# Kernel tuning notes

Hardware: AMD Instinct MI355X
Metric: run time of the kernel (lower is better)

Reference implementation:

```python
import jax, jax.numpy as jnp
import numpy as np

D = 768
H = 12
DH = D // H  # 64


def setup_inputs() -> dict:
    key = jax.random.key(0)
    ks = jax.random.split(key, 7)
    B, N = 16, 1024
    sequences = jax.random.normal(ks[0], (B, N, D), dtype=jnp.float32)
    s = 1.0 / np.sqrt(DH)
    # per-head torch Linear params: weight [out, in] = [DH, DH], bias [DH]
    Wq = jax.random.uniform(ks[1], (H, DH, DH), jnp.float32, -s, s)
    Wk = jax.random.uniform(ks[2], (H, DH, DH), jnp.float32, -s, s)
    Wv = jax.random.uniform(ks[3], (H, DH, DH), jnp.float32, -s, s)
    bq = jax.random.uniform(ks[4], (H, DH), jnp.float32, -s, s)
    bk = jax.random.uniform(ks[5], (H, DH), jnp.float32, -s, s)
    bv = jax.random.uniform(ks[6], (H, DH), jnp.float32, -s, s)
    return {"sequences": sequences, "Wq": Wq, "Wk": Wk, "Wv": Wv,
            "bq": bq, "bk": bk, "bv": bv}


def reference(sequences, Wq, Wk, Wv, bq, bk, bv):
    B, N, _ = sequences.shape
    x = sequences.reshape(B, N, H, DH)  # head slices of the feature dim
    # torch Linear: y = x @ W.T + b  -> einsum over the 'in' axis of W
    q = jnp.einsum('bnhd,hed->bnhe', x, Wq) + bq
    k = jnp.einsum('bnhd,hed->bnhe', x, Wk) + bk
    v = jnp.einsum('bnhd,hed->bnhe', x, Wv) + bv
    scores = jnp.einsum('bnhe,bmhe->bhnm', q, k) / jnp.sqrt(jnp.float32(DH))
    attn = jax.nn.softmax(scores, axis=-1)  # [B,H,N,N]
    out = jnp.einsum('bhnm,bmhe->bnhe', attn, v)
    return out.reshape(B, N, H * DH)  # hstack of per-head outputs
```

## Files before the change

### kernel.cpp

```cpp
#include <hip/hip_runtime.h>


#define NH 12
#define DHEAD 64
#define BB 16
#define NSEQ 1024
#define DMODEL 768
#define LSTR 72
#define QSCALE 0.18033688f

typedef unsigned short u16;
typedef unsigned int u32;
typedef u16 u16x8 __attribute__((ext_vector_type(8)));
typedef u16 u16x4 __attribute__((ext_vector_type(4)));
typedef __bf16 bf16x8 __attribute__((ext_vector_type(8)));
typedef float f32x4 __attribute__((ext_vector_type(4)));

union Frag { u16x8 u; bf16x8 b; };

__device__ __forceinline__ float fast_exp2(float x) {
#if __has_builtin(__builtin_amdgcn_exp2f)
    return __builtin_amdgcn_exp2f(x);
#else
    return exp2f(x);
#endif
}

__device__ __forceinline__ u16 f2bf(float f) {
    union { __bf16 h; u16 u; } c; c.h = (__bf16)f; return c.u;
}

__device__ __forceinline__ u16x8 cvt8(const float* __restrict__ p) {
    f32x4 a = *(const f32x4*)p;
    f32x4 b = *(const f32x4*)(p + 4);
    Frag r;
    r.b[0] = (__bf16)a[0]; r.b[1] = (__bf16)a[1]; r.b[2] = (__bf16)a[2]; r.b[3] = (__bf16)a[3];
    r.b[4] = (__bf16)b[0]; r.b[5] = (__bf16)b[1]; r.b[6] = (__bf16)b[2]; r.b[7] = (__bf16)b[3];
    return r.u;
}

__global__ __launch_bounds__(256) void wcvt_kernel(
    const float* __restrict__ Wq, const float* __restrict__ Wk,
    const float* __restrict__ Wv, u16* __restrict__ Wb)
{
    const int bx = blockIdx.x;
    const int m = bx / 24;
    const int off = (bx % 24) * 2048 + threadIdx.x * 8;
    const float* srcs[3] = { Wq, Wk, Wv };
    *(u16x8*)(Wb + m * 49152 + off) = cvt8(srcs[m] + off);
}

__global__ __launch_bounds__(256) void kv_kernel(
    const float* __restrict__ x,
    const u16*  __restrict__ Wb,
    const float* __restrict__ bk, const float* __restrict__ bv,
    u16* __restrict__ Ko,
    u16* __restrict__ Vt)
{
    __shared__ __align__(16) u16 w_lds[2][64 * LSTR];
    __shared__ __align__(16) u16 x_lds[128 * LSTR];

    const int bid = blockIdx.x;
    const int h     = bid % NH;
    const int chunk = (bid / NH) & 7;
    const int b     = bid / (NH * 8);

    const int t = threadIdx.x, lane = t & 63, wave = t >> 6;
    const int qd = lane >> 4, lm = lane & 15;

    {
        const int row = t >> 2, d0 = (t & 3) * 16;
#pragma unroll
        for (int m = 0; m < 2; m++) {
            const u16* s = Wb + (1 + m) * 49152 + h * 4096 + row * 64 + d0;
            *(u16x8*)&w_lds[m][row * LSTR + d0]     = *(const u16x8*)s;
            *(u16x8*)&w_lds[m][row * LSTR + d0 + 8] = *(const u16x8*)(s + 8);
        }
        const int xr = t >> 1, xd = (t & 1) * 32;
        const float* s = x + ((size_t)(b * NSEQ + chunk * 128 + xr)) * DMODEL + h * DHEAD + xd;
#pragma unroll
        for (int i = 0; i < 4; i++)
            *(u16x8*)&x_lds[xr * LSTR + xd + i * 8] = cvt8(s + i * 8);
    }
    __syncthreads();

    Frag xfrag[2][2];
#pragma unroll
    for (int mt = 0; mt < 2; mt++)
#pragma unroll
        for (int kk = 0; kk < 2; kk++)
            xfrag[mt][kk].u = *(const u16x8*)&x_lds[(wave * 32 + mt * 16 + lm) * LSTR + kk * 32 + qd * 8];

    u16* tx = &x_lds[wave * 32 * LSTR];
    const int key_base = chunk * 128 + wave * 32;

#pragma unroll
    for (int et = 0; et < 4; et++) {
        Frag wfrag[2];
#pragma unroll
        for (int kk = 0; kk < 2; kk++)
            wfrag[kk].u = *(const u16x8*)&w_lds[0][(et * 16 + lm) * LSTR + kk * 32 + qd * 8];
        f32x4 acc0 = {0.f,0.f,0.f,0.f}, acc1 = {0.f,0.f,0.f,0.f};
#pragma unroll
        for (int kk = 0; kk < 2; kk++) {
            acc0 = __builtin_amdgcn_mfma_f32_16x16x32_bf16(wfrag[kk].b, xfrag[0][kk].b, acc0, 0, 0, 0);
            acc1 = __builtin_amdgcn_mfma_f32_16x16x32_bf16(wfrag[kk].b, xfrag[1][kk].b, acc1, 0, 0, 0);
        }
        f32x4 b4 = *(const f32x4*)&bk[h * DHEAD + et * 16 + qd * 4];
        u16x4 o0, o1;
#pragma unroll
        for (int r = 0; r < 4; r++) {
            o0[r] = f2bf(acc0[r] + b4[r]);
            o1[r] = f2bf(acc1[r] + b4[r]);
        }
        *(u16x4*)&tx[lm * LSTR + et * 16 + qd * 4]        = o0;
        *(u16x4*)&tx[(16 + lm) * LSTR + et * 16 + qd * 4] = o1;
    }
    {
        const size_t base_out = ((size_t)(b * NH + h) * NSEQ + key_base) * DHEAD;
#pragma unroll
        for (int j = 0; j < 4; j++) {
            const int row = j * 8 + (lane >> 3), col = (lane & 7) * 8;
            u16x8 v = *(const u16x8*)&tx[row * LSTR + col];
            *(u16x8*)(Ko + base_out + (size_t)row * DHEAD + col) = v;
        }
    }

    const size_t vt_base = ((size_t)(b * NH + h)) * DHEAD * NSEQ;
#pragma unroll
    for (int et = 0; et < 4; et++) {
        Frag wvfrag[2];
#pragma unroll
        for (int kk = 0; kk < 2; kk++)
            wvfrag[kk].u = *(const u16x8*)&w_lds[1][(et * 16 + lm) * LSTR + kk * 32 + qd * 8];
        const float bvv = bv[h * DHEAD + et * 16 + lm];
#pragma unroll
        for (int mt = 0; mt < 2; mt++) {
            f32x4 acc = {0.f,0.f,0.f,0.f};
#pragma unroll
            for (int kk = 0; kk < 2; kk++)
                acc = __builtin_amdgcn_mfma_f32_16x16x32_bf16(xfrag[mt][kk].b, wvfrag[kk].b, acc, 0, 0, 0);
            u16x4 o;
#pragma unroll
            for (int r = 0; r < 4; r++) o[r] = f2bf(acc[r] + bvv);
            *(u16x4*)(Vt + vt_base + (size_t)(et * 16 + lm) * NSEQ + key_base + mt * 16 + qd * 4) = o;
        }
    }
}

__global__ __launch_bounds__(256, 2) void attn_kernel(
    const float* __restrict__ x, const u16* __restrict__ Wb,
    const float* __restrict__ bq,
    const u16* __restrict__ K, const u16* __restrict__ Vt,
    float* __restrict__ out)
{
    __shared__ __align__(16) u16 k_lds[64 * LSTR];
    __shared__ __align__(16) u16 vt_lds[64 * LSTR];
    __shared__ __align__(16) u16 p_lds[4][16 * LSTR];

    const int bid = blockIdx.x;
    const int bh = bid % 192;
    const int qt = bid / 192;
    const int h = bh % NH, b = bh / NH;

    const int t = threadIdx.x, lane = t & 63, wave = t >> 6;
    const int qd = lane >> 4, lm = lane & 15;
    const size_t bh_off = (size_t)bh * NSEQ * DHEAD;
    const int tb = qt * 256;

    {
        const int row = t >> 2, d0 = (t & 3) * 16;
        const u16* wq = Wb + h * 4096 + row * 64 + d0;
        *(u16x8*)&k_lds[row * LSTR + d0]     = *(const u16x8*)wq;
        *(u16x8*)&k_lds[row * LSTR + d0 + 8] = *(const u16x8*)(wq + 8);
    }
    __syncthreads();

    Frag qfrag[4][2];
    {
        const int xrow = lane >> 2, xd0 = (lane & 3) * 16;
#pragma unroll
        for (int mtl = 0; mtl < 4; mtl++) {
            const float* xs = x + ((size_t)(b * NSEQ + tb + wave * 64 + mtl * 16 + xrow)) * DMODEL
                              + h * DHEAD + xd0;
            *(u16x8*)&p_lds[wave][xrow * LSTR + xd0]     = cvt8(xs);
            *(u16x8*)&p_lds[wave][xrow * LSTR + xd0 + 8] = cvt8(xs + 8);
            Frag xB[2];
#pragma unroll
            for (int kk = 0; kk < 2; kk++)
                xB[kk].u = *(const u16x8*)&p_lds[wave][lm * LSTR + kk * 32 + qd * 8];
#pragma unroll
            for (int et = 0; et < 4; et++) {
                Frag wqA[2];
#pragma unroll
                for (int kk = 0; kk < 2; kk++)
                    wqA[kk].u = *(const u16x8*)&k_lds[(et * 16 + lm) * LSTR + kk * 32 + qd * 8];
                f32x4 acc = {0.f,0.f,0.f,0.f};
#pragma unroll
                for (int kk = 0; kk < 2; kk++)
                    acc = __builtin_amdgcn_mfma_f32_16x16x32_bf16(wqA[kk].b, xB[kk].b, acc, 0, 0, 0);
                f32x4 b4 = *(const f32x4*)&bq[h * DHEAD + et * 16 + qd * 4];
                u16x4 o;
#pragma unroll
                for (int r = 0; r < 4; r++) o[r] = f2bf((acc[r] + b4[r]) * QSCALE);
                *(u16x4*)&p_lds[wave][lm * LSTR + et * 16 + qd * 4] = o;
            }
#pragma unroll
            for (int kk = 0; kk < 2; kk++)
                qfrag[mtl][kk].u = *(const u16x8*)&p_lds[wave][lm * LSTR + kk * 32 + qd * 8];
        }
    }

    f32x4 o_acc[4][4] = {};
    f32x4 rsum = {0.f, 0.f, 0.f, 0.f};

    const u16* kb = K  + bh_off;
    const u16* vb = Vt + bh_off;

    const int srow = t >> 2, sd0 = (t & 3) * 16;

    u16x8 kreg0, kreg1, vreg0, vreg1;
    {
        const u16* sk = kb + (size_t)srow * DHEAD + sd0;
        kreg0 = *(const u16x8*)sk; kreg1 = *(const u16x8*)(sk + 8);
        const u16* sv = vb + (size_t)srow * NSEQ + sd0;
        vreg0 = *(const u16x8*)sv; vreg1 = *(const u16x8*)(sv + 8);
    }

#pragma unroll 1
    for (int it = 0; it < NSEQ / 64; it++) {
        __syncthreads();
        *(u16x8*)&k_lds[srow * LSTR + sd0]      = kreg0;
        *(u16x8*)&k_lds[srow * LSTR + sd0 + 8]  = kreg1;
        *(u16x8*)&vt_lds[srow * LSTR + sd0]     = vreg0;
        *(u16x8*)&vt_lds[srow * LSTR + sd0 + 8] = vreg1;
        __syncthreads();

        if (it + 1 < NSEQ / 64) {
            const u16* sk = kb + (size_t)((it + 1) * 64 + srow) * DHEAD + sd0;
            kreg0 = *(const u16x8*)sk; kreg1 = *(const u16x8*)(sk + 8);
            const u16* sv = vb + (size_t)srow * NSEQ + (it + 1) * 64 + sd0;
            vreg0 = *(const u16x8*)sv; vreg1 = *(const u16x8*)(sv + 8);
        }

        Frag kfrag[4][2];
#pragma unroll
        for (int kt = 0; kt < 4; kt++)
#pragma unroll
            for (int kk = 0; kk < 2; kk++)
                kfrag[kt][kk].u = *(const u16x8*)&k_lds[(kt * 16 + lm) * LSTR + kk * 32 + qd * 8];

        Frag pfrag[4][2];
#pragma unroll
        for (int mt = 0; mt < 4; mt++) {
            f32x4 st[4];
#pragma unroll
            for (int kt = 0; kt < 4; kt++) {
                f32x4 a = {0.f,0.f,0.f,0.f};
#pragma unroll
                for (int kk = 0; kk < 2; kk++)
                    a = __builtin_amdgcn_mfma_f32_16x16x32_bf16(kfrag[kt][kk].b, qfrag[mt][kk].b, a, 0, 0, 0);
                st[kt] = a;
            }
            float rs = 0.f;
#pragma unroll
            for (int kt = 0; kt < 4; kt++) {
                u16x4 pk;
#pragma unroll
                for (int r = 0; r < 4; r++) {
                    float p = fast_exp2(st[kt][r]);
                    rs += p;
                    pk[r] = f2bf(p);
                }
                *(u16x4*)&p_lds[wave][lm * LSTR + kt * 16 + qd * 4] = pk;
            }
            rsum[mt] += rs;
#pragma unroll
            for (int kk = 0; kk < 2; kk++)
                pfrag[mt][kk].u = *(const u16x8*)&p_lds[wave][lm * LSTR + kk * 32 + qd * 8];
        }

#pragma unroll
        for (int dt = 0; dt < 4; dt++) {
            Frag vfrag[2];
#pragma unroll
            for (int kk = 0; kk < 2; kk++)
                vfrag[kk].u = *(const u16x8*)&vt_lds[(dt * 16 + lm) * LSTR + kk * 32 + qd * 8];
#pragma unroll
            for (int kk = 0; kk < 2; kk++)
#pragma unroll
                for (int mt = 0; mt < 4; mt++)
                    o_acc[mt][dt] = __builtin_amdgcn_mfma_f32_16x16x32_bf16(pfrag[mt][kk].b, vfrag[kk].b, o_acc[mt][dt], 0, 0, 0);
        }
    }

#pragma unroll
    for (int mt = 0; mt < 4; mt++) {
        float s = rsum[mt];
        s += __shfl_xor(s, 16);
        s += __shfl_xor(s, 32);
        float inv = 1.f / s;
        float inv4[4];
#pragma unroll
        for (int r = 0; r < 4; r++) inv4[r] = __shfl(inv, qd * 4 + r);
#pragma unroll
        for (int dt = 0; dt < 4; dt++) {
            const int e = dt * 16 + lm;
#pragma unroll
            for (int r = 0; r < 4; r++) {
                const int n_tok = tb + wave * 64 + mt * 16 + qd * 4 + r;
                out[((size_t)(b * NSEQ + n_tok)) * DMODEL + h * DHEAD + e] =
                    o_acc[mt][dt][r] * inv4[r];
            }
        }
    }
}

extern "C" void kernel_launch(void* const* d_in, const int* in_sizes, int n_in,
                              void* d_out, int out_size, void* d_ws, size_t ws_size,
                              hipStream_t stream) {
    const float* x  = (const float*)d_in[0];
    const float* Wq = (const float*)d_in[1];
    const float* Wk = (const float*)d_in[2];
    const float* Wv = (const float*)d_in[3];
    const float* bq = (const float*)d_in[4];
    const float* bk = (const float*)d_in[5];
    const float* bv = (const float*)d_in[6];
    float* out = (float*)d_out;

    const size_t KV_ELEMS = (size_t)BB * NH * NSEQ * DHEAD;
    u16* Kw  = (u16*)d_ws;
    u16* Vtw = Kw + KV_ELEMS;
    u16* Wb  = Vtw + KV_ELEMS;

    wcvt_kernel<<<72, 256, 0, stream>>>(Wq, Wk, Wv, Wb);
    kv_kernel<<<BB * 8 * NH, 256, 0, stream>>>(x, Wb, bk, bv, Kw, Vtw);
    attn_kernel<<<(NSEQ / 256) * BB * NH, 256, 0, stream>>>(x, Wb, bq, Kw, Vtw, out);
}
```

Baseline: 96.83 us.

## Double-buffer K/V LDS, swizzle layout, and use permlane swaps instead of P round-trip

Replaces the padded single-buffer K/V shared-memory tiles with XOR-style swizzled, double-buffered tiles. This cuts the two barriers per iteration to one and lets loads for tile it+2 overlap compute on tile it. The P (softmax probabilities) and Q fragments are no longer written to and re-read from LDS. They are rearranged in registers with permlane32/permlane16 swap intrinsics, which removes the per-wave LDS scratch and its traffic. The cost is more LDS for double buffering, a dependency on the gfx950 permlane builtins, and a risk of getting the fragment lane mapping wrong.

After: 99.13 us. +2.4%, slower.

```diff
diff --git a/kernel.cpp b/kernel.cpp
--- a/kernel.cpp
+++ b/kernel.cpp
@@ -15,8 +15,9 @@
 typedef u16 u16x4 __attribute__((ext_vector_type(4)));
 typedef __bf16 bf16x8 __attribute__((ext_vector_type(8)));
 typedef float f32x4 __attribute__((ext_vector_type(4)));
-
-union Frag { u16x8 u; bf16x8 b; };
+typedef int i32x2 __attribute__((ext_vector_type(2)));
+
+union Frag { u16x8 u; bf16x8 b; u32 w[4]; };
 
 __device__ __forceinline__ float fast_exp2(float x) {
 #if __has_builtin(__builtin_amdgcn_exp2f)
@@ -28,6 +29,10 @@
 
 __device__ __forceinline__ u16 f2bf(float f) {
     union { __bf16 h; u16 u; } c; c.h = (__bf16)f; return c.u;
+}
+
+__device__ __forceinline__ u32 pk2(float lo, float hi) {
+    return (u32)f2bf(lo) | ((u32)f2bf(hi) << 16);
 }
 
 __device__ __forceinline__ u16x8 cvt8(const float* __restrict__ p) {
@@ -37,6 +42,16 @@
     r.b[0] = (__bf16)a[0]; r.b[1] = (__bf16)a[1]; r.b[2] = (__bf16)a[2]; r.b[3] = (__bf16)a[3];
     r.b[4] = (__bf16)b[0]; r.b[5] = (__bf16)b[1]; r.b[6] = (__bf16)b[2]; r.b[7] = (__bf16)b[3];
     return r.u;
+}
+
+__device__ __forceinline__ int sw(int row, int slot) {
+    return (row << 6) + (((slot + row) & 7) << 3);
+}
+
+__device__ __forceinline__ void lane4_shuffle(u32 a0, u32 a1, u32& wlo, u32& whi) {
+    i32x2 t = __builtin_amdgcn_permlane32_swap((int)a0, (int)a1, false, false);
+    i32x2 r = __builtin_amdgcn_permlane16_swap(t[0], t[1], false, false);
+    wlo = (u32)r[0]; whi = (u32)r[1];
 }
 
 __global__ __launch_bounds__(256) void wcvt_kernel(
@@ -154,9 +169,8 @@
     const u16* __restrict__ K, const u16* __restrict__ Vt,
     float* __restrict__ out)
 {
-    __shared__ __align__(16) u16 k_lds[64 * LSTR];
-    __shared__ __align__(16) u16 vt_lds[64 * LSTR];
-    __shared__ __align__(16) u16 p_lds[4][16 * LSTR];
+    __shared__ __align__(16) u16 k_lds[2][64 * 64];
+    __shared__ __align__(16) u16 v_lds[2][64 * 64];
 
     const int bid = blockIdx.x;
     const int bh = bid % 192;
@@ -168,87 +182,81 @@
     const size_t bh_off = (size_t)bh * NSEQ * DHEAD;
     const int tb = qt * 256;
 
-    {
-        const int row = t >> 2, d0 = (t & 3) * 16;
-        const u16* wq = Wb + h * 4096 + row * 64 + d0;
-        *(u16x8*)&k_lds[row * LSTR + d0]     = *(const u16x8*)wq;
-        *(u16x8*)&k_lds[row * LSTR + d0 + 8] = *(const u16x8*)(wq + 8);
+    const u16* kb = K  + bh_off;
+    const u16* vb = Vt + bh_off;
+
+    const int srow = t >> 2, sc = t & 3;
+
+    {
+        const u16* wq = Wb + h * 4096 + srow * 64 + sc * 16;
+        *(u16x8*)&k_lds[0][sw(srow, sc * 2)]     = *(const u16x8*)wq;
+        *(u16x8*)&k_lds[0][sw(srow, sc * 2 + 1)] = *(const u16x8*)(wq + 8);
+    }
+
+    u16x8 kreg0, kreg1, vreg0, vreg1;
+    {
+        const u16* sk = kb + (size_t)srow * DHEAD + sc * 16;
+        kreg0 = *(const u16x8*)sk; kreg1 = *(const u16x8*)(sk + 8);
+        const u16* sv = vb + (size_t)srow * NSEQ + sc * 16;
+        vreg0 = *(const u16x8*)sv; vreg1 = *(const u16x8*)(sv + 8);
     }
     __syncthreads();
 
     Frag qfrag[4][2];
-    {
-        const int xrow = lane >> 2, xd0 = (lane & 3) * 16;
-#pragma unroll
-        for (int mtl = 0; mtl < 4; mtl++) {
-            const float* xs = x + ((size_t)(b * NSEQ + tb + wave * 64 + mtl * 16 + xrow)) * DMODEL
-                              + h * DHEAD + xd0;
-            *(u16x8*)&p_lds[wave][xrow * LSTR + xd0]     = cvt8(xs);
-            *(u16x8*)&p_lds[wave][xrow * LSTR + xd0 + 8] = cvt8(xs + 8);
-            Frag xB[2];
-#pragma unroll
-            for (int kk = 0; kk < 2; kk++)
-                xB[kk].u = *(const u16x8*)&p_lds[wave][lm * LSTR + kk * 32 + qd * 8];
-#pragma unroll
-            for (int et = 0; et < 4; et++) {
-                Frag wqA[2];
-#pragma unroll
-                for (int kk = 0; kk < 2; kk++)
-                    wqA[kk].u = *(const u16x8*)&k_lds[(et * 16 + lm) * LSTR + kk * 32 + qd * 8];
-                f32x4 acc = {0.f,0.f,0.f,0.f};
-#pragma unroll
-                for (int kk = 0; kk < 2; kk++)
-                    acc = __builtin_amdgcn_mfma_f32_16x16x32_bf16(wqA[kk].b, xB[kk].b, acc, 0, 0, 0);
-                f32x4 b4 = *(const f32x4*)&bq[h * DHEAD + et * 16 + qd * 4];
-                u16x4 o;
-#pragma unroll
-                for (int r = 0; r < 4; r++) o[r] = f2bf((acc[r] + b4[r]) * QSCALE);
-                *(u16x4*)&p_lds[wave][lm * LSTR + et * 16 + qd * 4] = o;
-            }
-#pragma unroll
-            for (int kk = 0; kk < 2; kk++)
-                qfrag[mtl][kk].u = *(const u16x8*)&p_lds[wave][lm * LSTR + kk * 32 + qd * 8];
-        }
-    }
+#pragma unroll
+    for (int mtl = 0; mtl < 4; mtl++) {
+        const float* xs = x + ((size_t)(b * NSEQ + tb + wave * 64 + mtl * 16 + lm)) * DMODEL
+                          + h * DHEAD + qd * 8;
+        Frag xB[2];
+        xB[0].u = cvt8(xs);
+        xB[1].u = cvt8(xs + 32);
+        u32 Ap[4], Bp[4];
+#pragma unroll
+        for (int et = 0; et < 4; et++) {
+            Frag wqA[2];
+#pragma unroll
+            for (int kk = 0; kk < 2; kk++)
+                wqA[kk].u = *(const u16x8*)&k_lds[0][sw(et * 16 + lm, kk * 4 + qd)];
+            f32x4 acc = {0.f,0.f,0.f,0.f};
+#pragma unroll
+            for (int kk = 0; kk < 2; kk++)
+                acc = __builtin_amdgcn_mfma_f32_16x16x32_bf16(wqA[kk].b, xB[kk].b, acc, 0, 0, 0);
+            f32x4 b4 = *(const f32x4*)&bq[h * DHEAD + et * 16 + qd * 4];
+            Ap[et] = pk2((acc[0] + b4[0]) * QSCALE, (acc[1] + b4[1]) * QSCALE);
+            Bp[et] = pk2((acc[2] + b4[2]) * QSCALE, (acc[3] + b4[3]) * QSCALE);
+        }
+#pragma unroll
+        for (int kk = 0; kk < 2; kk++) {
+            lane4_shuffle(Ap[2 * kk], Ap[2 * kk + 1], qfrag[mtl][kk].w[0], qfrag[mtl][kk].w[2]);
+            lane4_shuffle(Bp[2 * kk], Bp[2 * kk + 1], qfrag[mtl][kk].w[1], qfrag[mtl][kk].w[3]);
+        }
+    }
+
+    *(u16x8*)&k_lds[1][sw(srow, sc * 2)]     = kreg0;
+    *(u16x8*)&k_lds[1][sw(srow, sc * 2 + 1)] = kreg1;
+    *(u16x8*)&v_lds[1][sw(srow, sc * 2)]     = vreg0;
+    *(u16x8*)&v_lds[1][sw(srow, sc * 2 + 1)] = vreg1;
+    {
+        const u16* sk = kb + (size_t)(64 + srow) * DHEAD + sc * 16;
+        kreg0 = *(const u16x8*)sk; kreg1 = *(const u16x8*)(sk + 8);
+        const u16* sv = vb + (size_t)srow * NSEQ + 64 + sc * 16;
+        vreg0 = *(const u16x8*)sv; vreg1 = *(const u16x8*)(sv + 8);
+    }
+    __syncthreads();
 
     f32x4 o_acc[4][4] = {};
     f32x4 rsum = {0.f, 0.f, 0.f, 0.f};
 
-    const u16* kb = K  + bh_off;
-    const u16* vb = Vt + bh_off;
-
-    const int srow = t >> 2, sd0 = (t & 3) * 16;
-
-    u16x8 kreg0, kreg1, vreg0, vreg1;
-    {
-        const u16* sk = kb + (size_t)srow * DHEAD + sd0;
-        kreg0 = *(const u16x8*)sk; kreg1 = *(const u16x8*)(sk + 8);
-        const u16* sv = vb + (size_t)srow * NSEQ + sd0;
-        vreg0 = *(const u16x8*)sv; vreg1 = *(const u16x8*)(sv + 8);
-    }
-
 #pragma unroll 1
     for (int it = 0; it < NSEQ / 64; it++) {
-        __syncthreads();
-        *(u16x8*)&k_lds[srow * LSTR + sd0]      = kreg0;
-        *(u16x8*)&k_lds[srow * LSTR + sd0 + 8]  = kreg1;
-        *(u16x8*)&vt_lds[srow * LSTR + sd0]     = vreg0;
-        *(u16x8*)&vt_lds[srow * LSTR + sd0 + 8] = vreg1;
-        __syncthreads();
-
-        if (it + 1 < NSEQ / 64) {
-            const u16* sk = kb + (size_t)((it + 1) * 64 + srow) * DHEAD + sd0;
-            kreg0 = *(const u16x8*)sk; kreg1 = *(const u16x8*)(sk + 8);
-            const u16* sv = vb + (size_t)srow * NSEQ + (it + 1) * 64 + sd0;
-            vreg0 = *(const u16x8*)sv; vreg1 = *(const u16x8*)(sv + 8);
-        }
+        const int cur = 1 - (it & 1);
 
         Frag kfrag[4][2];
 #pragma unroll
         for (int kt = 0; kt < 4; kt++)
 #pragma unroll
             for (int kk = 0; kk < 2; kk++)
-                kfrag[kt][kk].u = *(const u16x8*)&k_lds[(kt * 16 + lm) * LSTR + kk * 32 + qd * 8];
+                kfrag[kt][kk].u = *(const u16x8*)&k_lds[cur][sw(kt * 16 + lm, kk * 4 + qd)];
 
         Frag pfrag[4][2];
 #pragma unroll
@@ -263,21 +271,22 @@
                 st[kt] = a;
             }
             float rs = 0.f;
+            u32 Ap[4], Bp[4];
 #pragma unroll
             for (int kt = 0; kt < 4; kt++) {
-                u16x4 pk;
-#pragma unroll
-                for (int r = 0; r < 4; r++) {
-                    float p = fast_exp2(st[kt][r]);
-                    rs += p;
-                    pk[r] = f2bf(p);
-                }
-                *(u16x4*)&p_lds[wave][lm * LSTR + kt * 16 + qd * 4] = pk;
+                float e0 = fast_exp2(st[kt][0]);
+                float e1 = fast_exp2(st[kt][1]);
+                float e2 = fast_exp2(st[kt][2]);
+                float e3 = fast_exp2(st[kt][3]);
+                rs += (e0 + e1) + (e2 + e3);
+                Ap[kt] = pk2(e0, e1); Bp[kt] = pk2(e2, e3);
             }
             rsum[mt] += rs;
 #pragma unroll
-            for (int kk = 0; kk < 2; kk++)
-                pfrag[mt][kk].u = *(const u16x8*)&p_lds[wave][lm * LSTR + kk * 32 + qd * 8];
+            for (int kk = 0; kk < 2; kk++) {
+                lane4_shuffle(Ap[2 * kk], Ap[2 * kk + 1], pfrag[mt][kk].w[0], pfrag[mt][kk].w[2]);
+                lane4_shuffle(Bp[2 * kk], Bp[2 * kk + 1], pfrag[mt][kk].w[1], pfrag[mt][kk].w[3]);
+            }
         }
 
 #pragma unroll
@@ -285,13 +294,27 @@
             Frag vfrag[2];
 #pragma unroll
             for (int kk = 0; kk < 2; kk++)
-                vfrag[kk].u = *(const u16x8*)&vt_lds[(dt * 16 + lm) * LSTR + kk * 32 + qd * 8];
+                vfrag[kk].u = *(const u16x8*)&v_lds[cur][sw(dt * 16 + lm, kk * 4 + qd)];
 #pragma unroll
             for (int kk = 0; kk < 2; kk++)
 #pragma unroll
                 for (int mt = 0; mt < 4; mt++)
                     o_acc[mt][dt] = __builtin_amdgcn_mfma_f32_16x16x32_bf16(pfrag[mt][kk].b, vfrag[kk].b, o_acc[mt][dt], 0, 0, 0);
         }
+
+        if (it < NSEQ / 64 - 1) {
+            *(u16x8*)&k_lds[1 - cur][sw(srow, sc * 2)]     = kreg0;
+            *(u16x8*)&k_lds[1 - cur][sw(srow, sc * 2 + 1)] = kreg1;
+            *(u16x8*)&v_lds[1 - cur][sw(srow, sc * 2)]     = vreg0;
+            *(u16x8*)&v_lds[1 - cur][sw(srow, sc * 2 + 1)] = vreg1;
+        }
+        if (it < NSEQ / 64 - 2) {
+            const u16* sk = kb + (size_t)((it + 2) * 64 + srow) * DHEAD + sc * 16;
+            kreg0 = *(const u16x8*)sk; kreg1 = *(const u16x8*)(sk + 8);
+            const u16* sv = vb + (size_t)srow * NSEQ + (it + 2) * 64 + sc * 16;
+            vreg0 = *(const u16x8*)sv; vreg1 = *(const u16x8*)(sv + 8);
+        }
+        __syncthreads();
     }
 
 #pragma unroll
```
